# Kernel tuning notes

Measured on AMD Instinct MI355X. Metric: run time of the kernel, lower is better.

Reference implementation:

```python
import jax, jax.numpy as jnp
import numpy as np

NUM_ITER = 10
DIM = 512
SPATIAL = 28 * 28  # 784


def sqrt_newton_schulz(A, num_iter=NUM_ITER):
    # A: [B, D, D] SPD-ish bilinear matrix
    B, D = A.shape[0], A.shape[1]
    norm_A = jnp.sqrt(jnp.sum(A * A, axis=(1, 2)))  # Frobenius norm, [B]
    norm_A3 = norm_A[:, None, None]
    Y = A / norm_A3
    I = jnp.broadcast_to(jnp.eye(D, dtype=A.dtype), (B, D, D))
    Z = I
    for _ in range(num_iter):
        T = 0.5 * (3.0 * I - jnp.matmul(Z, Y))
        Y = jnp.matmul(Y, T)
        Z = jnp.matmul(T, Z)
    return Y * jnp.sqrt(norm_A)[:, None, None]


def setup_inputs() -> dict:
    key = jax.random.key(0)
    k1, k2 = jax.random.split(key)
    X = jax.random.normal(k1, (64, DIM, 28, 28), dtype=jnp.float32)
    fc_weight = jax.random.normal(k2, (200, DIM * DIM), dtype=jnp.float32) * 0.01
    fc_bias = jnp.zeros((200,), dtype=jnp.float32)
    return {"X": X, "fc_weight": fc_weight, "fc_bias": fc_bias}


def reference(X, fc_weight, fc_bias):
    B = X.shape[0]
    x = X.reshape(B, DIM, SPATIAL)                      # [B, 512, 784]
    A = jnp.einsum('bip,bjp->bij', x, x) / SPATIAL      # bilinear pooling [B,512,512]
    Y = sqrt_newton_schulz(A, NUM_ITER)                 # matrix square root
    v = Y.reshape(B, DIM * DIM)
    v = jnp.sign(v) * jnp.sqrt(jnp.abs(v) + 1e-5)       # signed sqrt
    n = jnp.sqrt(jnp.sum(v * v, axis=1, keepdims=True))
    v = v / jnp.maximum(n, 1e-12)                       # L2 normalize (F.normalize)
    return v @ fc_weight.T + fc_bias                    # [B, 200]
```

## Files before the change

kernel.cpp:

```cpp
#include <hip/hip_runtime.h>
#include <math.h>
#include <stdint.h>

#define DIMM 512
#define SLOT_S 262144

typedef __attribute__((ext_vector_type(8))) _Float16 half8v;
typedef __attribute__((ext_vector_type(8))) unsigned short ushort8v;
typedef __attribute__((ext_vector_type(4))) float f32x4;

__device__ __forceinline__ unsigned short f2h(float f) {
    _Float16 h = (_Float16)f;
    return __builtin_bit_cast(unsigned short, h);
}
__device__ __forceinline__ float h2f(unsigned short u) {
    return (float)__builtin_bit_cast(_Float16, u);
}
__device__ __forceinline__ float sgn_sqrt(float tv)
{
    float r = sqrtf(fabsf(tv) + 1e-5f);
    return tv > 0.f ? r : (tv < 0.f ? -r : 0.f);
}

__global__ __launch_bounds__(256) void ns_single(
    const unsigned short* __restrict__ A0, const unsigned short* __restrict__ A1,
    const unsigned short* __restrict__ Bb,
    unsigned short* __restrict__ C0, unsigned short* __restrict__ C1,
    int lda, long aslot, int ldb, long bslot, int K, int nz)
{
    __shared__ __align__(16) unsigned short sm[8960];

    const int nwg = gridDim.x;
    const int chunk = nwg >> 3;
    const int bid = blockIdx.x;
    const int wu = (bid & 7) * chunk + (bid >> 3);
    const int per_batch = nz * 10;
    const int bz = wu / per_batch;
    const int rr = wu - bz * per_batch;
    const int z  = rr / 10;
    const int tile = rr - z * 10;
    int ti, tj;
    if (tile < 4)      { ti = 0; tj = tile; }
    else if (tile < 7) { ti = 1; tj = tile - 3; }
    else if (tile < 9) { ti = 2; tj = tile - 5; }
    else               { ti = 3; tj = 3; }

    const unsigned short* A  = (z ? A1 : A0) + (size_t)bz * aslot;
    const unsigned short* Bp = Bb + (size_t)bz * bslot;
    unsigned short* C = (z ? C1 : C0) + (size_t)bz * SLOT_S;

    const int m0 = ti * 128;
    const int n0 = tj * 128;

    const int t = threadIdx.x;
    const int l = t & 63;
    const int w = t >> 6;
    const int wr = w >> 1, wc = w & 1;
    const int lr = l & 15;
    const int sc = (((l >> 4) ^ ((l >> 1) & 3)) << 3);

    const int sr = t >> 1, sh = t & 1;
    const int swz = (sr >> 1) & 3;
    const int slot0 = ((((sh << 1) | 0) ^ swz) << 3);
    const int slot1 = ((((sh << 1) | 1) ^ swz) << 3);
    const int wbase = sr * 32;
    const unsigned short* pA = A  + (size_t)(m0 + sr) * lda + sh * 16;
    const unsigned short* pB = Bp + (size_t)(n0 + sr) * ldb + sh * 16;

    f32x4 acc[4][4] = {};

    ushort8v a0, a1, b0, b1;
#define LOADALL(OFF) do { \
    a0 = *(const ushort8v*)(pA + (OFF));  a1 = *(const ushort8v*)(pA + (OFF) + 8); \
    b0 = *(const ushort8v*)(pB + (OFF));  b1 = *(const ushort8v*)(pB + (OFF) + 8); \
  } while (0)

    LOADALL(0);
    const int nsteps = K >> 5;
    for (int s = 0; s < nsteps; ++s) {
        __syncthreads();
        *(ushort8v*)&sm[       wbase + slot0] = a0; *(ushort8v*)&sm[       wbase + slot1] = a1;
        *(ushort8v*)&sm[4096 + wbase + slot0] = b0; *(ushort8v*)&sm[4096 + wbase + slot1] = b1;
        __syncthreads();
        if (s + 1 < nsteps) LOADALL((s + 1) * 32);

        half8v ah[4], bh[4];
#pragma unroll
        for (int f = 0; f < 4; ++f) {
            const int ra = ((wr * 64 + f * 16 + lr) << 5) + sc;
            const int rb = ((wc * 64 + f * 16 + lr) << 5) + sc;
            ah[f] = *(const half8v*)(&sm[ra]);
            bh[f] = *(const half8v*)(&sm[4096 + rb]);
        }
#pragma unroll
        for (int fm = 0; fm < 4; ++fm)
#pragma unroll
            for (int fn = 0; fn < 4; ++fn)
                acc[fm][fn] = __builtin_amdgcn_mfma_f32_16x16x32_f16(ah[fm], bh[fn], acc[fm][fn], 0, 0, 0);
    }
#undef LOADALL

#pragma unroll
    for (int fm = 0; fm < 4; ++fm) {
#pragma unroll
        for (int j = 0; j < 4; ++j) {
            const int row = m0 + wr * 64 + fm * 16 + (l >> 4) * 4 + j;
            const unsigned short* arow = A + (size_t)row * lda;
            const size_t crow = (size_t)row * 512;
#pragma unroll
            for (int fn = 0; fn < 4; ++fn) {
                const int col = n0 + wc * 64 + fn * 16 + lr;
                float v = 1.5f * h2f(arow[col]) - 0.5f * acc[fm][fn][j];
                acc[fm][fn][j] = v;
                C[crow + col] = f2h(v);
            }
        }
    }

    if (ti != tj) {
        const int TP = 70;
        unsigned short* smT = sm;
        const int cst = wc * 64 + lr;
        const int r4  = (l >> 4) * 4;
        const int rc2 = t >> 1;
        const int chh = t & 1;
        __syncthreads();
#pragma unroll
        for (int h = 0; h < 2; ++h) {
            if (wr == h) {
#pragma unroll
                for (int fm = 0; fm < 4; ++fm) {
#pragma unroll
                    for (int fn = 0; fn < 4; ++fn) {
                        ushort4 q;
                        q.x = f2h(acc[fm][fn][0]);
                        q.y = f2h(acc[fm][fn][1]);
                        q.z = f2h(acc[fm][fn][2]);
                        q.w = f2h(acc[fm][fn][3]);
                        *(ushort4*)&smT[(cst + fn * 16) * TP + r4 + fm * 16] = q;
                    }
                }
            }
            __syncthreads();
            {
                unsigned short* dst = C + (size_t)(n0 + rc2) * 512 + m0 + h * 64 + chh * 32;
                const unsigned short* srcp = &smT[rc2 * TP + chh * 32];
#pragma unroll
                for (int k = 0; k < 8; ++k)
                    *(ushort4*)(dst + k * 4) = *(const ushort4*)(srcp + k * 4);
            }
            __syncthreads();
        }
    }
}

__global__ __launch_bounds__(256) void gram_single(const float* __restrict__ X,
                                                   unsigned short* __restrict__ C0,
                                                   float alpha, int K)
{
    __shared__ __align__(16) unsigned short sm[8960];

    const int nwg = gridDim.x;
    const int chunk = nwg >> 3;
    const int wu = (blockIdx.x & 7) * chunk + (blockIdx.x >> 3);
    const int bz = wu / 10, tile = wu - bz * 10;
    int ti, tj;
    if (tile < 4)      { ti = 0; tj = tile; }
    else if (tile < 7) { ti = 1; tj = tile - 3; }
    else if (tile < 9) { ti = 2; tj = tile - 5; }
    else               { ti = 3; tj = 3; }
    const int m0 = ti * 128, n0 = tj * 128;
    unsigned short* C = C0 + (size_t)bz * SLOT_S;

    const int t = threadIdx.x;
    const int l = t & 63;
    const int w = t >> 6;
    const int wr = w >> 1, wc = w & 1;
    const int lr = l & 15;
    const int sc = (((l >> 4) ^ ((l >> 1) & 3)) << 3);

    const int sr = t >> 1, sh = t & 1;
    const int swz = (sr >> 1) & 3;
    const int slot0 = ((((sh << 1) | 0) ^ swz) << 3);
    const int slot1 = ((((sh << 1) | 1) ^ swz) << 3);
    const int wbase = sr * 32;

    const float* pXa = X + ((size_t)bz * 512 + m0 + sr) * 784 + sh * 16;
    const float* pXb = X + ((size_t)bz * 512 + n0 + sr) * 784 + sh * 16;

    f32x4 acc[4][4] = {};

    float4 xa0, xa1, xa2, xa3, xb0, xb1, xb2, xb3;
    ushort8v a0, a1, b0, b1;

#define GLD(OFF) do { \
    if ((OFF) + sh * 16 < 784) { \
        xa0 = *(const float4*)(pXa + (OFF));      xa1 = *(const float4*)(pXa + (OFF) + 4); \
        xa2 = *(const float4*)(pXa + (OFF) + 8);  xa3 = *(const float4*)(pXa + (OFF) + 12); \
        xb0 = *(const float4*)(pXb + (OFF));      xb1 = *(const float4*)(pXb + (OFF) + 4); \
        xb2 = *(const float4*)(pXb + (OFF) + 8);  xb3 = *(const float4*)(pXb + (OFF) + 12); \
    } else { \
        xa0 = xa1 = xa2 = xa3 = make_float4(0.f, 0.f, 0.f, 0.f); \
        xb0 = xb1 = xb2 = xb3 = make_float4(0.f, 0.f, 0.f, 0.f); \
    } } while (0)

#define CV8(F0, F1, O) do { \
    (O)[0] = f2h((F0).x); (O)[1] = f2h((F0).y); \
    (O)[2] = f2h((F0).z); (O)[3] = f2h((F0).w); \
    (O)[4] = f2h((F1).x); (O)[5] = f2h((F1).y); \
    (O)[6] = f2h((F1).z); (O)[7] = f2h((F1).w); \
  } while (0)

#define CONVALL() do { \
    CV8(xa0, xa1, a0); CV8(xa2, xa3, a1); \
    CV8(xb0, xb1, b0); CV8(xb2, xb3, b1); \
  } while (0)

    GLD(0);
    CONVALL();
    const int nsteps = K >> 5;
    for (int s = 0; s < nsteps; ++s) {
        __syncthreads();
        *(ushort8v*)&sm[       wbase + slot0] = a0; *(ushort8v*)&sm[       wbase + slot1] = a1;
        *(ushort8v*)&sm[4096 + wbase + slot0] = b0; *(ushort8v*)&sm[4096 + wbase + slot1] = b1;
        __syncthreads();
        if (s + 1 < nsteps) GLD((s + 1) * 32);

        half8v ah[4], bh[4];
#pragma unroll
        for (int f = 0; f < 4; ++f) {
            const int ra = ((wr * 64 + f * 16 + lr) << 5) + sc;
            const int rb = ((wc * 64 + f * 16 + lr) << 5) + sc;
            ah[f] = *(const half8v*)(&sm[ra]);
            bh[f] = *(const half8v*)(&sm[4096 + rb]);
        }
#pragma unroll
        for (int fm = 0; fm < 4; ++fm)
#pragma unroll
            for (int fn = 0; fn < 4; ++fn)
                acc[fm][fn] = __builtin_amdgcn_mfma_f32_16x16x32_f16(ah[fm], bh[fn], acc[fm][fn], 0, 0, 0);
        if (s + 1 < nsteps) CONVALL();
    }
#undef GLD
#undef CV8
#undef CONVALL

#pragma unroll
    for (int fm = 0; fm < 4; ++fm) {
#pragma unroll
        for (int j = 0; j < 4; ++j) {
            const int row = m0 + wr * 64 + fm * 16 + (l >> 4) * 4 + j;
            const size_t crow = (size_t)row * 512;
#pragma unroll
            for (int fn = 0; fn < 4; ++fn) {
                const int col = n0 + wc * 64 + fn * 16 + lr;
                float v = acc[fm][fn][j] * alpha;
                acc[fm][fn][j] = v;
                C[crow + col] = f2h(v);
            }
        }
    }

    if (ti != tj) {
        const int TP = 70;
        unsigned short* smT = sm;
        const int cst = wc * 64 + lr;
        const int r4  = (l >> 4) * 4;
        const int rc2 = t >> 1;
        const int chh = t & 1;
        __syncthreads();
#pragma unroll
        for (int h = 0; h < 2; ++h) {
            if (wr == h) {
#pragma unroll
                for (int fm = 0; fm < 4; ++fm) {
#pragma unroll
                    for (int fn = 0; fn < 4; ++fn) {
                        ushort4 q;
                        q.x = f2h(acc[fm][fn][0]);
                        q.y = f2h(acc[fm][fn][1]);
                        q.z = f2h(acc[fm][fn][2]);
                        q.w = f2h(acc[fm][fn][3]);
                        *(ushort4*)&smT[(cst + fn * 16) * TP + r4 + fm * 16] = q;
                    }
                }
            }
            __syncthreads();
            {
                unsigned short* dst = C + (size_t)(n0 + rc2) * 512 + m0 + h * 64 + chh * 32;
                const unsigned short* srcp = &smT[rc2 * TP + chh * 32];
#pragma unroll
                for (int k = 0; k < 8; ++k)
                    *(ushort4*)(dst + k * 4) = *(const ushort4*)(srcp + k * 4);
            }
            __syncthreads();
        }
    }
}

__global__ __launch_bounds__(256) void frob_s(const unsigned short* __restrict__ P,
                                              float* __restrict__ pp)
{
    const int b = blockIdx.x >> 3, sg = blockIdx.x & 7;
    const unsigned short* p = P + (size_t)b * SLOT_S + sg * 32768;
    float s = 0.f;
    for (int i = threadIdx.x * 8; i < 32768; i += 2048) {
        ushort8v h = *(const ushort8v*)(p + i);
#pragma unroll
        for (int j = 0; j < 8; ++j) {
            float v = h2f(h[j]);
            s += v * v;
        }
    }
    __shared__ float red[256];
    red[threadIdx.x] = s;
    __syncthreads();
    for (int wd = 128; wd > 0; wd >>= 1) {
        if (threadIdx.x < wd) red[threadIdx.x] += red[threadIdx.x + wd];
        __syncthreads();
    }
    if (threadIdx.x == 0) pp[blockIdx.x] = red[0];
}

__global__ __launch_bounds__(64) void frob_fin(const float* __restrict__ pp,
                                               float* __restrict__ out)
{
    const int b = threadIdx.x;
    float s = 0.f;
#pragma unroll
    for (int i = 0; i < 8; ++i) s += pp[b * 8 + i];
    out[b] = sqrtf(s);
}

__global__ __launch_bounds__(256) void init_s(const unsigned short* __restrict__ A,
                                              unsigned short* __restrict__ Y,
                                              const float* __restrict__ norm)
{
    const int total = 64 * 32768;
    for (int g = blockIdx.x * 256 + threadIdx.x; g < total; g += gridDim.x * 256) {
        const int b = g >> 15;
        const int off = (g & 32767) * 8;
        const float rn = 1.0f / norm[b];
        ushort8v h = *(const ushort8v*)(A + (size_t)b * SLOT_S + off);
        ushort8v o;
#pragma unroll
        for (int j = 0; j < 8; ++j) o[j] = f2h(h2f(h[j]) * rn);
        *(ushort8v*)(Y + (size_t)b * SLOT_S + off) = o;
    }
}

__global__ __launch_bounds__(256) void ssqrt_s(const unsigned short* __restrict__ Yf,
                                               unsigned short* __restrict__ Vp,
                                               const float* __restrict__ norm)
{
    const int total = 64 * 32768;
    for (int g = blockIdx.x * 256 + threadIdx.x; g < total; g += gridDim.x * 256) {
        const int b = g >> 15;
        const int off = (g & 32767) * 8;
        const float s = sqrtf(norm[b]);
        ushort8v h = *(const ushort8v*)(Yf + (size_t)b * SLOT_S + off);
        ushort8v o;
#pragma unroll
        for (int j = 0; j < 8; ++j) o[j] = f2h(sgn_sqrt(h2f(h[j]) * s));
        *(ushort8v*)(Vp + (size_t)b * SLOT_S + off) = o;
    }
}

__global__ __launch_bounds__(256) void fc_mfma_s(
    const unsigned short* __restrict__ Vp, const float* __restrict__ Wfc,
    float* __restrict__ part)
{
    __shared__ __align__(16) unsigned short sm2[6144];

    const int sp = blockIdx.x >> 1;
    const int nt = blockIdx.x & 1;
    const int kbase = sp * 2048;
    const int n0 = nt * 128;

    const int t = threadIdx.x;
    const int l = t & 63;
    const int w = t >> 6;
    const int wr = w >> 1, wc = w & 1;
    const int lr = l & 15;
    const int sc = (((l >> 4) ^ ((l >> 1) & 3)) << 3);

    const int sr = t >> 1, sh = t & 1;
    const int swz = (sr >> 1) & 3;
    const int slot0 = ((((sh << 1) | 0) ^ swz) << 3);
    const int slot1 = ((((sh << 1) | 1) ^ swz) << 3);

    const unsigned short* gA = Vp + (size_t)sr * SLOT_S + kbase + sh * 16;
    const int wrow = n0 + sr;
    const bool wv = wrow < 200;
    const float* gB = Wfc + (size_t)wrow * 262144 + kbase + sh * 16;

    f32x4 acc[2][4] = {};

    ushort8v va0, va1, vb0, vb1;
    float4 wf0, wf1, wf2, wf3;
#define FLOAD(OFF) do { \
    if (t < 128) { \
        va0 = *(const ushort8v*)(gA + (OFF)); va1 = *(const ushort8v*)(gA + (OFF) + 8); \
    } \
    if (wv) { \
        wf0 = *(const float4*)(gB + (OFF));      wf1 = *(const float4*)(gB + (OFF) + 4); \
        wf2 = *(const float4*)(gB + (OFF) + 8);  wf3 = *(const float4*)(gB + (OFF) + 12); \
    } else { \
        wf0 = wf1 = wf2 = wf3 = make_float4(0.f, 0.f, 0.f, 0.f); \
    } \
    vb0[0] = f2h(wf0.x); vb0[1] = f2h(wf0.y); vb0[2] = f2h(wf0.z); vb0[3] = f2h(wf0.w); \
    vb0[4] = f2h(wf1.x); vb0[5] = f2h(wf1.y); vb0[6] = f2h(wf1.z); vb0[7] = f2h(wf1.w); \
    vb1[0] = f2h(wf2.x); vb1[1] = f2h(wf2.y); vb1[2] = f2h(wf2.z); vb1[3] = f2h(wf2.w); \
    vb1[4] = f2h(wf3.x); vb1[5] = f2h(wf3.y); vb1[6] = f2h(wf3.z); vb1[7] = f2h(wf3.w); \
  } while (0)

    FLOAD(0);
    for (int s = 0; s < 64; ++s) {
        __syncthreads();
        if (t < 128) {
            *(ushort8v*)&sm2[(sr << 5) + slot0] = va0;
            *(ushort8v*)&sm2[(sr << 5) + slot1] = va1;
        }
        *(ushort8v*)&sm2[2048 + (sr << 5) + slot0] = vb0;
        *(ushort8v*)&sm2[2048 + (sr << 5) + slot1] = vb1;
        __syncthreads();
        if (s + 1 < 64) FLOAD((s + 1) * 32);

        half8v ah[2], bh[4];
#pragma unroll
        for (int f = 0; f < 2; ++f) {
            const int ra = ((wr * 32 + f * 16 + lr) << 5) + sc;
            ah[f] = *(const half8v*)(&sm2[ra]);
        }
#pragma unroll
        for (int f = 0; f < 4; ++f) {
            const int rb = ((wc * 64 + f * 16 + lr) << 5) + sc;
            bh[f] = *(const half8v*)(&sm2[2048 + rb]);
        }
#pragma unroll
        for (int fm = 0; fm < 2; ++fm)
#pragma unroll
            for (int fn = 0; fn < 4; ++fn)
                acc[fm][fn] = __builtin_amdgcn_mfma_f32_16x16x32_f16(ah[fm], bh[fn], acc[fm][fn], 0, 0, 0);
    }
#undef FLOAD

    float* pb = part + (size_t)(sp * 2 + nt) * 64 * 128;
#pragma unroll
    for (int fm = 0; fm < 2; ++fm)
#pragma unroll
        for (int j = 0; j < 4; ++j) {
            const int row = wr * 32 + fm * 16 + (l >> 4) * 4 + j;
#pragma unroll
            for (int fn = 0; fn < 4; ++fn) {
                const int col = wc * 64 + fn * 16 + lr;
                pb[(size_t)row * 128 + col] = acc[fm][fn][j];
            }
        }
}

__global__ __launch_bounds__(256) void fc_reduce(
    const float* __restrict__ part, const float* __restrict__ n2,
    const float* __restrict__ bias, float* __restrict__ out)
{
    const int p = blockIdx.x * 256 + threadIdx.x;
    if (p >= 64 * 200) return;
    const int b = p / 200, o = p % 200;
    const int nt = o >> 7, n = o & 127;
    float s = 0.f;
    for (int c = 0; c < 128; ++c)
        s += part[((size_t)(c * 2 + nt) * 64 + b) * 128 + n];
    const float nb = fmaxf(n2[b], 1e-12f);
    out[p] = s / nb + bias[o];
}

extern "C" void kernel_launch(void* const* d_in, const int* in_sizes, int n_in,
                              void* d_out, int out_size, void* d_ws, size_t ws_size,
                              hipStream_t stream)
{
    const float* X    = (const float*)d_in[0];
    const float* Wfc  = (const float*)d_in[1];
    const float* bias = (const float*)d_in[2];
    float* out = (float*)d_out;

    float* norm  = (float*)d_ws;
    float* norm2 = norm + 64;
    float* fpart = norm2 + 64;
    float* part  = fpart + 512;
    unsigned short* region = (unsigned short*)(part + (size_t)256 * 64 * 128);

    unsigned short* P[4];
    for (int i = 0; i < 4; ++i) P[i] = region + (size_t)i * 64 * SLOT_S;

    gram_single<<<640, 256, 0, stream>>>(X, P[0], 1.0f / 784.0f, 800);
    frob_s<<<512, 256, 0, stream>>>(P[0], fpart);
    frob_fin<<<1, 64, 0, stream>>>(fpart, norm);
    init_s<<<1024, 256, 0, stream>>>(P[0], P[1], norm);

    ns_single<<<640, 256, 0, stream>>>(P[1], P[1], P[1], P[2], P[2],
        512, (long)SLOT_S, 512, (long)SLOT_S, 512, 1);
    ns_single<<<640, 256, 0, stream>>>(P[2], P[2], P[1], P[3], P[3],
        512, (long)SLOT_S, 512, (long)SLOT_S, 512, 1);

    unsigned short *Y = P[2], *M = P[3], *F0 = P[0], *F1 = P[1];
    for (int it = 1; it <= 8; ++it) {
        ns_single<<<1280, 256, 0, stream>>>(M, Y, M, F0, F1,
            512, (long)SLOT_S, 512, (long)SLOT_S, 512, 2);
        ns_single<<<640, 256, 0, stream>>>(F0, F0, M, Y, Y,
            512, (long)SLOT_S, 512, (long)SLOT_S, 512, 1);
        unsigned short* Mold = M;
        M = Y;
        Y = F1;
        F1 = Mold;
    }
    ns_single<<<640, 256, 0, stream>>>(Y, Y, M, F0, F0,
        512, (long)SLOT_S, 512, (long)SLOT_S, 512, 1);

    unsigned short* Vp = F1;
    ssqrt_s<<<1024, 256, 0, stream>>>(F0, Vp, norm);
    frob_s<<<512, 256, 0, stream>>>(Vp, fpart);
    frob_fin<<<1, 64, 0, stream>>>(fpart, norm2);
    fc_mfma_s<<<dim3(256), 256, 0, stream>>>(Vp, Wfc, part);
    fc_reduce<<<50, 256, 0, stream>>>(part, norm2, bias, out);
}
```

Measured before the change: 994.4 us.

## Fold NS affine update into B operand and fuse init/signed-sqrt into GEMMs

After: 994.1 us. Within noise of the previous version (-0.0%).

```diff
diff --git a/kernel.cpp b/kernel.cpp
--- a/kernel.cpp
+++ b/kernel.cpp
@@ -26,7 +26,8 @@
     const unsigned short* __restrict__ A0, const unsigned short* __restrict__ A1,
     const unsigned short* __restrict__ Bb,
     unsigned short* __restrict__ C0, unsigned short* __restrict__ C1,
-    int lda, long aslot, int ldb, long bslot, int K, int nz)
+    int lda, long aslot, int ldb, long bslot, int K,
+    int mode, const float* __restrict__ norm, int nz)
 {
     __shared__ __align__(16) unsigned short sm[8960];
 
@@ -49,6 +50,15 @@
     const unsigned short* Bp = Bb + (size_t)bz * bslot;
     unsigned short* C = (z ? C1 : C0) + (size_t)bz * SLOT_S;
 
+    float rn = 1.0f, sq = 0.0f;
+    if (mode != 0) {
+        const float nv = norm[bz];
+        rn = 1.0f / nv;
+        sq = sqrtf(nv);
+    }
+    const _Float16 bscale = (_Float16)((mode == 1 || mode == 2) ? (-0.5f * rn) : -0.5f);
+    const float csc = (mode == 1) ? rn : 1.0f;
+
     const int m0 = ti * 128;
     const int n0 = tj * 128;
 
@@ -66,6 +76,7 @@
     const int wbase = sr * 32;
     const unsigned short* pA = A  + (size_t)(m0 + sr) * lda + sh * 16;
     const unsigned short* pB = Bp + (size_t)(n0 + sr) * ldb + sh * 16;
+    const int dbase = (n0 + sr) - sh * 16;
 
     f32x4 acc[4][4] = {};
 
@@ -75,14 +86,29 @@
     b0 = *(const ushort8v*)(pB + (OFF));  b1 = *(const ushort8v*)(pB + (OFF) + 8); \
   } while (0)
 
+#define CONVB(S) do { \
+    half8v bv0 = __builtin_bit_cast(half8v, b0); \
+    half8v bv1 = __builtin_bit_cast(half8v, b1); \
+    bv0 *= bscale; bv1 *= bscale; \
+    const int dj = dbase - (S) * 32; \
+    _Pragma("unroll") \
+    for (int j = 0; j < 8; ++j) { \
+        if (dj == j)     bv0[j] += (_Float16)1.5f; \
+        if (dj == j + 8) bv1[j] += (_Float16)1.5f; \
+    } \
+    b0 = __builtin_bit_cast(ushort8v, bv0); \
+    b1 = __builtin_bit_cast(ushort8v, bv1); \
+  } while (0)
+
     LOADALL(0);
+    CONVB(0);
     const int nsteps = K >> 5;
     for (int s = 0; s < nsteps; ++s) {
         __syncthreads();
         *(ushort8v*)&sm[       wbase + slot0] = a0; *(ushort8v*)&sm[       wbase + slot1] = a1;
         *(ushort8v*)&sm[4096 + wbase + slot0] = b0; *(ushort8v*)&sm[4096 + wbase + slot1] = b1;
         __syncthreads();
-        if (s + 1 < nsteps) LOADALL((s + 1) * 32);
+        if (s + 1 < nsteps) { LOADALL((s + 1) * 32); CONVB(s + 1); }
 
         half8v ah[4], bh[4];
 #pragma unroll
@@ -99,18 +125,19 @@
                 acc[fm][fn] = __builtin_amdgcn_mfma_f32_16x16x32_f16(ah[fm], bh[fn], acc[fm][fn], 0, 0, 0);
     }
 #undef LOADALL
+#undef CONVB
 
 #pragma unroll
     for (int fm = 0; fm < 4; ++fm) {
 #pragma unroll
         for (int j = 0; j < 4; ++j) {
             const int row = m0 + wr * 64 + fm * 16 + (l >> 4) * 4 + j;
-            const unsigned short* arow = A + (size_t)row * lda;
             const size_t crow = (size_t)row * 512;
 #pragma unroll
             for (int fn = 0; fn < 4; ++fn) {
                 const int col = n0 + wc * 64 + fn * 16 + lr;
-                float v = 1.5f * h2f(arow[col]) - 0.5f * acc[fm][fn][j];
+                float v = csc * acc[fm][fn][j];
+                if (mode == 3) v = sgn_sqrt(v * sq);
                 acc[fm][fn][j] = v;
                 C[crow + col] = f2h(v);
             }
@@ -330,40 +357,6 @@
 #pragma unroll
     for (int i = 0; i < 8; ++i) s += pp[b * 8 + i];
     out[b] = sqrtf(s);
-}
-
-__global__ __launch_bounds__(256) void init_s(const unsigned short* __restrict__ A,
-                                              unsigned short* __restrict__ Y,
-                                              const float* __restrict__ norm)
-{
-    const int total = 64 * 32768;
-    for (int g = blockIdx.x * 256 + threadIdx.x; g < total; g += gridDim.x * 256) {
-        const int b = g >> 15;
-        const int off = (g & 32767) * 8;
-        const float rn = 1.0f / norm[b];
-        ushort8v h = *(const ushort8v*)(A + (size_t)b * SLOT_S + off);
-        ushort8v o;
-#pragma unroll
-        for (int j = 0; j < 8; ++j) o[j] = f2h(h2f(h[j]) * rn);
-        *(ushort8v*)(Y + (size_t)b * SLOT_S + off) = o;
-    }
-}
-
-__global__ __launch_bounds__(256) void ssqrt_s(const unsigned short* __restrict__ Yf,
-                                               unsigned short* __restrict__ Vp,
-                                               const float* __restrict__ norm)
-{
-    const int total = 64 * 32768;
-    for (int g = blockIdx.x * 256 + threadIdx.x; g < total; g += gridDim.x * 256) {
-        const int b = g >> 15;
-        const int off = (g & 32767) * 8;
-        const float s = sqrtf(norm[b]);
-        ushort8v h = *(const ushort8v*)(Yf + (size_t)b * SLOT_S + off);
-        ushort8v o;
-#pragma unroll
-        for (int j = 0; j < 8; ++j) o[j] = f2h(sgn_sqrt(h2f(h[j]) * s));
-        *(ushort8v*)(Vp + (size_t)b * SLOT_S + off) = o;
-    }
 }
 
 __global__ __launch_bounds__(256) void fc_mfma_s(
@@ -495,29 +488,27 @@
     gram_single<<<640, 256, 0, stream>>>(X, P[0], 1.0f / 784.0f, 800);
     frob_s<<<512, 256, 0, stream>>>(P[0], fpart);
     frob_fin<<<1, 64, 0, stream>>>(fpart, norm);
-    init_s<<<1024, 256, 0, stream>>>(P[0], P[1], norm);
-
-    ns_single<<<640, 256, 0, stream>>>(P[1], P[1], P[1], P[2], P[2],
-        512, (long)SLOT_S, 512, (long)SLOT_S, 512, 1);
-    ns_single<<<640, 256, 0, stream>>>(P[2], P[2], P[1], P[3], P[3],
-        512, (long)SLOT_S, 512, (long)SLOT_S, 512, 1);
+
+    ns_single<<<640, 256, 0, stream>>>(P[0], P[0], P[0], P[2], P[2],
+        512, (long)SLOT_S, 512, (long)SLOT_S, 512, 1, norm, 1);
+    ns_single<<<640, 256, 0, stream>>>(P[2], P[2], P[0], P[3], P[3],
+        512, (long)SLOT_S, 512, (long)SLOT_S, 512, 2, norm, 1);
 
     unsigned short *Y = P[2], *M = P[3], *F0 = P[0], *F1 = P[1];
     for (int it = 1; it <= 8; ++it) {
         ns_single<<<1280, 256, 0, stream>>>(M, Y, M, F0, F1,
-            512, (long)SLOT_S, 512, (long)SLOT_S, 512, 2);
+            512, (long)SLOT_S, 512, (long)SLOT_S, 512, 0, norm, 2);
         ns_single<<<640, 256, 0, stream>>>(F0, F0, M, Y, Y,
-            512, (long)SLOT_S, 512, (long)SLOT_S, 512, 1);
+            512, (long)SLOT_S, 512, (long)SLOT_S, 512, 0, norm, 1);
         unsigned short* Mold = M;
         M = Y;
         Y = F1;
         F1 = Mold;
     }
     ns_single<<<640, 256, 0, stream>>>(Y, Y, M, F0, F0,
-        512, (long)SLOT_S, 512, (long)SLOT_S, 512, 1);
-
-    unsigned short* Vp = F1;
-    ssqrt_s<<<1024, 256, 0, stream>>>(F0, Vp, norm);
+        512, (long)SLOT_S, 512, (long)SLOT_S, 512, 3, norm, 1);
+
+    unsigned short* Vp = F0;
     frob_s<<<512, 256, 0, stream>>>(Vp, fpart);
     frob_fin<<<1, 64, 0, stream>>>(fpart, norm2);
     fc_mfma_s<<<dim3(256), 256, 0, stream>>>(Vp, Wfc, part);
```
